# Optimization experiments

Hardware: AMD Instinct MI355X
Metric: run time of the kernel (lower is better)

The kernel has to match this reference:

```python
import jax, jax.numpy as jnp
import numpy as np

INPUT_SIZE = 64
HIDDEN = 1024
SEQ_LEN = 256
BATCH = 128
TARGET_LEN = 96


def lstm_cell(x, h, c, Wih, Whh, bih, bhh):
    # x: [B, in], h/c: [B, H]; torch gate order: i, f, g, o
    z = x @ Wih.T + h @ Whh.T + bih + bhh  # [B, 4H]
    i, f, g, o = jnp.split(z, 4, axis=-1)
    c_new = jax.nn.sigmoid(f) * c + jax.nn.sigmoid(i) * jnp.tanh(g)
    h_new = jax.nn.sigmoid(o) * jnp.tanh(c_new)
    return h_new, c_new


def setup_inputs() -> dict:
    key = jax.random.key(0)
    ks = jax.random.split(key, 12)
    s_in = 1.0 / np.sqrt(HIDDEN)  # torch LSTM init scale ~ U(-1/sqrt(H), 1/sqrt(H))
    def u(k, shape):
        return jax.random.uniform(k, shape, jnp.float32, -s_in, s_in)
    return {
        "input_batch": jax.random.normal(ks[0], (SEQ_LEN, BATCH, INPUT_SIZE), jnp.float32),
        "target_batch": jax.random.normal(ks[1], (TARGET_LEN, BATCH, INPUT_SIZE), jnp.float32),
        "enc_Wih": u(ks[2], (4 * HIDDEN, INPUT_SIZE)),
        "enc_Whh": u(ks[3], (4 * HIDDEN, HIDDEN)),
        "enc_bih": u(ks[4], (4 * HIDDEN,)),
        "enc_bhh": u(ks[5], (4 * HIDDEN,)),
        "dec_Wih": u(ks[6], (4 * HIDDEN, INPUT_SIZE)),
        "dec_Whh": u(ks[7], (4 * HIDDEN, HIDDEN)),
        "dec_bih": u(ks[8], (4 * HIDDEN,)),
        "dec_bhh": u(ks[9], (4 * HIDDEN,)),
        "lin_W": u(ks[10], (INPUT_SIZE, HIDDEN)),
        "lin_b": u(ks[11], (INPUT_SIZE,)),
    }


def reference(input_batch, target_batch, enc_Wih, enc_Whh, enc_bih, enc_bhh,
              dec_Wih, dec_Whh, dec_bih, dec_bhh, lin_W, lin_b):
    B = input_batch.shape[1]
    h0 = jnp.zeros((B, HIDDEN), input_batch.dtype)
    c0 = jnp.zeros((B, HIDDEN), input_batch.dtype)

    # ---- encoder: LSTM over seq_len ----
    def enc_step(carry, x_t):
        h, c = carry
        h, c = lstm_cell(x_t, h, c, enc_Wih, enc_Whh, enc_bih, enc_bhh)
        return (h, c), None
    (h_enc, c_enc), _ = jax.lax.scan(enc_step, (h0, c0), input_batch)

    # ---- decoder: recursive (no teacher forcing), target_len steps ----
    def dec_step(carry, _):
        x, h, c = carry
        h, c = lstm_cell(x, h, c, dec_Wih, dec_Whh, dec_bih, dec_bhh)
        y = h @ lin_W.T + lin_b  # [B, input_size]
        return (y, h, c), y
    x0 = input_batch[-1]  # [B, input_size]
    _, outputs = jax.lax.scan(dec_step, (x0, h_enc, c_enc), None, length=TARGET_LEN)
    return outputs  # [target_len, B, input_size]
```

## Files before the change

### kernel.cpp

```cpp
#include <hip/hip_runtime.h>
#include <stdint.h>

#define IN    64
#define H     1024
#define G4    4096
#define BATCH 128
#define SEQ   256
#define TLEN  96
#define KCAT  1088
#define NSTEP (SEQ + TLEN)
#define NBLK  256
#define HPAD  1032
#define ZPAD  132

typedef __attribute__((ext_vector_type(8))) short bf16x8;
typedef __attribute__((ext_vector_type(4))) float f32x4;

__device__ __forceinline__ unsigned short f2bf(float f) {
  union { float f; uint32_t u; } v; v.f = f;
  uint32_t u = v.u;
  return (unsigned short)((u + 0x7fffu + ((u >> 16) & 1u)) >> 16);
}

__device__ __forceinline__ void gload_lds16_sc0(const unsigned short* g, unsigned short* l) {
  __builtin_amdgcn_global_load_lds((const __attribute__((address_space(1))) unsigned int*)g,
                                   (__attribute__((address_space(3))) unsigned int*)l, 16, 0, 1);
}

__global__ void k_convert(const float* __restrict__ src, unsigned short* __restrict__ dst, int n) {
  int i = blockIdx.x * blockDim.x + threadIdx.x;
  int stride = gridDim.x * blockDim.x;
  for (; i < n; i += stride) dst[i] = f2bf(src[i]);
}

__global__ void k_pack(const float* __restrict__ Wih, const float* __restrict__ Whh,
                       const float* __restrict__ bih, const float* __restrict__ bhh,
                       unsigned short* __restrict__ Wcat, float* __restrict__ bcat) {
  int p = blockIdx.x;
  int j = p >> 2, g = p & 3;
  int r = g * H + j;
  for (int c = threadIdx.x; c < KCAT; c += blockDim.x) {
    float v = (c < IN) ? Wih[r * IN + c] : Whh[r * H + (c - IN)];
    Wcat[(size_t)p * KCAT + c] = f2bf(v);
  }
  if (threadIdx.x == 0) bcat[p] = bih[r] + bhh[r];
}

__global__ void k_deceff(const float* __restrict__ Wih, const float* __restrict__ Whh,
                         const float* __restrict__ bih, const float* __restrict__ bhh,
                         const float* __restrict__ lin, const float* __restrict__ linb,
                         unsigned short* __restrict__ Weff, float* __restrict__ beff) {
  int p = blockIdx.x;
  int j = p >> 2, g = p & 3;
  int r = g * H + j;
  __shared__ float wr[IN];
  if (threadIdx.x < IN) wr[threadIdx.x] = Wih[r * IN + threadIdx.x];
  __syncthreads();
  for (int k = threadIdx.x; k < H; k += blockDim.x) {
    float acc = Whh[(size_t)r * H + k];
    #pragma unroll 8
    for (int i = 0; i < IN; ++i) acc += wr[i] * lin[(size_t)i * H + k];
    Weff[(size_t)p * H + k] = f2bf(acc);
  }
  if (threadIdx.x == 0) {
    float s = bih[r] + bhh[r];
    for (int i = 0; i < IN; ++i) s += wr[i] * linb[i];
    beff[p] = s;
  }
}

__global__ __launch_bounds__(512, 2) void k_lstm(
    const unsigned short* __restrict__ xin,
    const unsigned short* __restrict__ Wenc,  const float* __restrict__ benc,
    const unsigned short* __restrict__ Wdec0, const float* __restrict__ bdec0,
    const unsigned short* __restrict__ Wdeff, const float* __restrict__ bdeff,
    unsigned short* __restrict__ hbuf, unsigned short* __restrict__ hhist,
    unsigned int* __restrict__ flags, unsigned int* __restrict__ tickets)
{
  extern __shared__ char smem[];
  unsigned short* hs = (unsigned short*)smem;
  float*          zs = (float*)(smem + 16 * HPAD * 2);
  __shared__ int s_xcd, s_slot;
  const int tid  = threadIdx.x;
  const int lane = tid & 63;
  const int wave = tid >> 6;
  if (tid == 0) {
    unsigned x;
    asm volatile("s_getreg_b32 %0, hwreg(HW_REG_XCC_ID)" : "=s"(x));
    x &= 7;
    unsigned tk = __hip_atomic_fetch_add(&tickets[x], 1u, __ATOMIC_RELAXED, __HIP_MEMORY_SCOPE_AGENT);
    s_xcd = (int)x; s_slot = (int)(tk & 31);
  }
  __syncthreads();
  const int grp  = s_xcd;
  const int slot = s_slot;
  const int m0   = grp * 16;
  const int n0   = slot * 128;
  const int gw   = n0 + wave * 16;
  const int fm   = lane & 15;
  const int fk   = (lane >> 4) * 8;
  const int crow = tid >> 5;
  const int ul   = tid & 31;
  const unsigned int* myflags = flags + (size_t)grp * 32;

  bf16x8 B[34];
  float cst = 0.f;
  int p = 0;
  for (int t = 0; t < NSTEP; ++t) {
    const bool is_enc = (t < SEQ);
    if (t == 0 || t == SEQ) {
      const unsigned short* W = (t == 0) ? Wenc : Wdec0;
      const unsigned short* wr = W + (size_t)(gw + fm) * KCAT + fk;
      #pragma unroll
      for (int kt = 0; kt < 32; ++kt) B[kt] = *(const bf16x8*)(wr + IN + kt * 32);
      B[32] = *(const bf16x8*)(wr);
      B[33] = *(const bf16x8*)(wr + 32);
    } else if (t == SEQ + 1) {
      const unsigned short* wr = Wdeff + (size_t)(gw + fm) * H + fk;
      #pragma unroll
      for (int kt = 0; kt < 32; ++kt) B[kt] = *(const bf16x8*)(wr + kt * 32);
    }
    const float* bias = is_enc ? benc : (t == SEQ ? bdec0 : bdeff);
    const unsigned short* xsrc =
        is_enc ? xin + (size_t)t * BATCH * IN
               : (t == SEQ ? xin + (size_t)(SEQ - 1) * BATCH * IN : nullptr);
    if (t > 0) {
      const unsigned short* hb = hbuf + (size_t)p * BATCH * H + (size_t)m0 * H;
      #pragma unroll
      for (int j = 0; j < 4; ++j) {
        int row  = wave * 2 + (j >> 1);
        int half = (j & 1) * 512;
        gload_lds16_sc0(hb + (size_t)row * H + half + lane * 8, &hs[row * HPAD + half]);
      }
    }
    __syncthreads();
    f32x4 acc = {0.f, 0.f, 0.f, 0.f};
    if (t > 0) {
      const unsigned short* as = &hs[fm * HPAD + fk];
      #pragma unroll
      for (int kt = 0; kt < 32; ++kt)
        acc = __builtin_amdgcn_mfma_f32_16x16x32_bf16(*(const bf16x8*)(as + kt * 32), B[kt], acc, 0, 0, 0);
    }
    if (xsrc) {
      const unsigned short* xa = xsrc + (size_t)(m0 + fm) * IN + fk;
      acc = __builtin_amdgcn_mfma_f32_16x16x32_bf16(*(const bf16x8*)(xa),      B[32], acc, 0, 0, 0);
      acc = __builtin_amdgcn_mfma_f32_16x16x32_bf16(*(const bf16x8*)(xa + 32), B[33], acc, 0, 0, 0);
    }
    {
      int colz = wave * 16 + fm;
      int rb   = (lane >> 4) * 4;
      #pragma unroll
      for (int j = 0; j < 4; ++j) zs[(rb + j) * ZPAD + colz] = acc[j];
    }
    __syncthreads();
    {
      const float4 z4 = *(const float4*)&zs[crow * ZPAD + 4 * ul];
      const float4 b4 = *(const float4*)&bias[n0 + 4 * ul];
      float zi = z4.x + b4.x, zf = z4.y + b4.y, zg = z4.z + b4.z, zo = z4.w + b4.w;
      float gi = 1.f / (1.f + __expf(-zi));
      float gf = 1.f / (1.f + __expf(-zf));
      float gg = tanhf(zg);
      float go = 1.f / (1.f + __expf(-zo));
      float c  = gf * cst + gi * gg;
      cst = c;
      float h = go * tanhf(c);
      unsigned short hb16 = f2bf(h);
      size_t idx = (size_t)(m0 + crow) * H + (n0 >> 2) + ul;
      hbuf[(size_t)(1 - p) * BATCH * H + idx] = hb16;
      if (!is_enc) hhist[(size_t)(t - SEQ) * BATCH * H + idx] = hb16;
    }
    p ^= 1;
    if (t + 1 < NSTEP) {
      __syncthreads();
      if (tid == 0)
        __hip_atomic_store(&flags[grp * 32 + slot], (unsigned)(t + 1),
                           __ATOMIC_RELAXED, __HIP_MEMORY_SCOPE_AGENT);
      if (tid < 32) {
        while (__hip_atomic_load(&myflags[tid], __ATOMIC_RELAXED, __HIP_MEMORY_SCOPE_AGENT) < (unsigned)(t + 1))
          __builtin_amdgcn_s_sleep(1);
      }
      __syncthreads();
    }
  }
}

__global__ __launch_bounds__(256) void k_out(
    const unsigned short* __restrict__ hhist, const unsigned short* __restrict__ linb16,
    const float* __restrict__ linb, float* __restrict__ out)
{
  const int tid  = threadIdx.x;
  const int lane = tid & 63;
  const int wave = tid >> 6;
  const int fm   = lane & 15;
  const int fk   = (lane >> 4) * 8;
  const int R0   = blockIdx.x * 64 + wave * 16;
  f32x4 acc[4] = {{0.f,0.f,0.f,0.f},{0.f,0.f,0.f,0.f},{0.f,0.f,0.f,0.f},{0.f,0.f,0.f,0.f}};
  const unsigned short* ha = hhist + (size_t)(R0 + fm) * H + fk;
  #pragma unroll 2
  for (int kc = 0; kc < H; kc += 32) {
    bf16x8 a = *(const bf16x8*)(ha + kc);
    #pragma unroll
    for (int nq = 0; nq < 4; ++nq) {
      bf16x8 b = *(const bf16x8*)(linb16 + (size_t)(nq * 16 + fm) * H + fk + kc);
      acc[nq] = __builtin_amdgcn_mfma_f32_16x16x32_bf16(a, b, acc[nq], 0, 0, 0);
    }
  }
  #pragma unroll
  for (int nq = 0; nq < 4; ++nq) {
    int col = nq * 16 + fm;
    float bb = linb[col];
    #pragma unroll
    for (int j = 0; j < 4; ++j) {
      int R = R0 + (lane >> 4) * 4 + j;
      out[(size_t)R * IN + col] = acc[nq][j] + bb;
    }
  }
}

extern "C" void kernel_launch(void* const* d_in, const int* in_sizes, int n_in,
                              void* d_out, int out_size, void* d_ws, size_t ws_size,
                              hipStream_t stream) {
  const float* input_batch = (const float*)d_in[0];
  const float* eWih = (const float*)d_in[2];
  const float* eWhh = (const float*)d_in[3];
  const float* ebih = (const float*)d_in[4];
  const float* ebhh = (const float*)d_in[5];
  const float* dWih = (const float*)d_in[6];
  const float* dWhh = (const float*)d_in[7];
  const float* dbih = (const float*)d_in[8];
  const float* dbhh = (const float*)d_in[9];
  const float* linW = (const float*)d_in[10];
  const float* linb = (const float*)d_in[11];
  float* out = (float*)d_out;

  char* ws = (char*)d_ws;
  size_t off = 0;
  auto alloc = [&](size_t bytes) -> void* {
    void* pp = ws + off;
    off = (off + bytes + 255) & ~(size_t)255;
    return pp;
  };
  unsigned short* xin   = (unsigned short*)alloc((size_t)SEQ * BATCH * IN * 2);
  unsigned short* Wenc  = (unsigned short*)alloc((size_t)G4 * KCAT * 2);
  float*          benc  = (float*)         alloc((size_t)G4 * 4);
  unsigned short* Wdec0 = (unsigned short*)alloc((size_t)G4 * KCAT * 2);
  float*          bdec0 = (float*)         alloc((size_t)G4 * 4);
  unsigned short* Wdeff = (unsigned short*)alloc((size_t)G4 * H * 2);
  float*          bdeff = (float*)         alloc((size_t)G4 * 4);
  unsigned short* linbf = (unsigned short*)alloc((size_t)IN * H * 2);
  unsigned short* hbuf  = (unsigned short*)alloc((size_t)2 * BATCH * H * 2);
  unsigned short* hhist = (unsigned short*)alloc((size_t)TLEN * BATCH * H * 2);
  unsigned int*   flags = (unsigned int*)  alloc((size_t)8 * 32 * sizeof(unsigned));
  unsigned int*   tickets = (unsigned int*)alloc((size_t)8 * sizeof(unsigned));
  (void)ws_size; (void)in_sizes; (void)n_in; (void)out_size;

  hipMemsetAsync(flags, 0, (size_t)8 * 32 * sizeof(unsigned), stream);
  hipMemsetAsync(tickets, 0, (size_t)8 * sizeof(unsigned), stream);
  hipLaunchKernelGGL(k_convert, dim3(512), dim3(256), 0, stream, input_batch, xin, SEQ * BATCH * IN);
  hipLaunchKernelGGL(k_convert, dim3(64),  dim3(256), 0, stream, linW, linbf, IN * H);
  hipLaunchKernelGGL(k_pack,   dim3(G4), dim3(256), 0, stream, eWih, eWhh, ebih, ebhh, Wenc, benc);
  hipLaunchKernelGGL(k_pack,   dim3(G4), dim3(256), 0, stream, dWih, dWhh, dbih, dbhh, Wdec0, bdec0);
  hipLaunchKernelGGL(k_deceff, dim3(G4), dim3(256), 0, stream, dWih, dWhh, dbih, dbhh, linW, linb, Wdeff, bdeff);

  void* args[] = { &xin, &Wenc, &benc, &Wdec0, &bdec0, &Wdeff, &bdeff, &hbuf, &hhist, &flags, &tickets };
  hipLaunchCooperativeKernel((void*)k_lstm, dim3(NBLK), dim3(512), args, 86016, stream);

  hipLaunchKernelGGL(k_out, dim3((TLEN * BATCH) / 64), dim3(256), 0, stream, hhist, linbf, linb, out);
}
```

Measured before the change: 4.322 ms.

## Swap MFMA operands so each lane holds all four gates, drop z LDS staging

```diff
diff --git a/kernel.cpp b/kernel.cpp
--- a/kernel.cpp
+++ b/kernel.cpp
@@ -11,7 +11,6 @@
 #define NSTEP (SEQ + TLEN)
 #define NBLK  256
 #define HPAD  1032
-#define ZPAD  132
 
 typedef __attribute__((ext_vector_type(8))) short bf16x8;
 typedef __attribute__((ext_vector_type(4))) float f32x4;
@@ -79,7 +78,7 @@
 {
   extern __shared__ char smem[];
   unsigned short* hs = (unsigned short*)smem;
-  float*          zs = (float*)(smem + 16 * HPAD * 2);
+  __shared__ unsigned short ht[16][40];
   __shared__ int s_xcd, s_slot;
   const int tid  = threadIdx.x;
   const int lane = tid & 63;
@@ -98,12 +97,15 @@
   const int n0   = slot * 128;
   const int gw   = n0 + wave * 16;
   const int fm   = lane & 15;
-  const int fk   = (lane >> 4) * 8;
-  const int crow = tid >> 5;
-  const int ul   = tid & 31;
+  const int fku  = lane >> 4;
+  const int fk   = fku * 8;
+  const int unit = slot * 32 + wave * 4 + fku;
+  const int hrow = tid >> 5;
+  const int hcol = tid & 31;
   const unsigned int* myflags = flags + (size_t)grp * 32;
 
   bf16x8 B[34];
+  float4 bias4;
   float cst = 0.f;
   int p = 0;
   for (int t = 0; t < NSTEP; ++t) {
@@ -120,7 +122,10 @@
       #pragma unroll
       for (int kt = 0; kt < 32; ++kt) B[kt] = *(const bf16x8*)(wr + kt * 32);
     }
-    const float* bias = is_enc ? benc : (t == SEQ ? bdec0 : bdeff);
+    if (t == 0 || t == SEQ || t == SEQ + 1) {
+      const float* bptr = (t == 0) ? benc : (t == SEQ ? bdec0 : bdeff);
+      bias4 = *(const float4*)&bptr[4 * unit];
+    }
     const unsigned short* xsrc =
         is_enc ? xin + (size_t)t * BATCH * IN
                : (t == SEQ ? xin + (size_t)(SEQ - 1) * BATCH * IN : nullptr);
@@ -134,29 +139,26 @@
       }
     }
     __syncthreads();
-    f32x4 acc = {0.f, 0.f, 0.f, 0.f};
+    f32x4 acc0 = {0.f, 0.f, 0.f, 0.f};
+    f32x4 acc1 = {0.f, 0.f, 0.f, 0.f};
     if (t > 0) {
       const unsigned short* as = &hs[fm * HPAD + fk];
       #pragma unroll
-      for (int kt = 0; kt < 32; ++kt)
-        acc = __builtin_amdgcn_mfma_f32_16x16x32_bf16(*(const bf16x8*)(as + kt * 32), B[kt], acc, 0, 0, 0);
+      for (int kt = 0; kt < 32; kt += 2) {
+        acc0 = __builtin_amdgcn_mfma_f32_16x16x32_bf16(B[kt],     *(const bf16x8*)(as + kt * 32),      acc0, 0, 0, 0);
+        acc1 = __builtin_amdgcn_mfma_f32_16x16x32_bf16(B[kt + 1], *(const bf16x8*)(as + kt * 32 + 32), acc1, 0, 0, 0);
+      }
     }
     if (xsrc) {
       const unsigned short* xa = xsrc + (size_t)(m0 + fm) * IN + fk;
-      acc = __builtin_amdgcn_mfma_f32_16x16x32_bf16(*(const bf16x8*)(xa),      B[32], acc, 0, 0, 0);
-      acc = __builtin_amdgcn_mfma_f32_16x16x32_bf16(*(const bf16x8*)(xa + 32), B[33], acc, 0, 0, 0);
+      acc0 = __builtin_amdgcn_mfma_f32_16x16x32_bf16(B[32], *(const bf16x8*)(xa),      acc0, 0, 0, 0);
+      acc1 = __builtin_amdgcn_mfma_f32_16x16x32_bf16(B[33], *(const bf16x8*)(xa + 32), acc1, 0, 0, 0);
     }
     {
-      int colz = wave * 16 + fm;
-      int rb   = (lane >> 4) * 4;
-      #pragma unroll
-      for (int j = 0; j < 4; ++j) zs[(rb + j) * ZPAD + colz] = acc[j];
-    }
-    __syncthreads();
-    {
-      const float4 z4 = *(const float4*)&zs[crow * ZPAD + 4 * ul];
-      const float4 b4 = *(const float4*)&bias[n0 + 4 * ul];
-      float zi = z4.x + b4.x, zf = z4.y + b4.y, zg = z4.z + b4.z, zo = z4.w + b4.w;
+      float zi = acc0[0] + acc1[0] + bias4.x;
+      float zf = acc0[1] + acc1[1] + bias4.y;
+      float zg = acc0[2] + acc1[2] + bias4.z;
+      float zo = acc0[3] + acc1[3] + bias4.w;
       float gi = 1.f / (1.f + __expf(-zi));
       float gf = 1.f / (1.f + __expf(-zf));
       float gg = tanhf(zg);
@@ -164,10 +166,14 @@
       float c  = gf * cst + gi * gg;
       cst = c;
       float h = go * tanhf(c);
-      unsigned short hb16 = f2bf(h);
-      size_t idx = (size_t)(m0 + crow) * H + (n0 >> 2) + ul;
-      hbuf[(size_t)(1 - p) * BATCH * H + idx] = hb16;
-      if (!is_enc) hhist[(size_t)(t - SEQ) * BATCH * H + idx] = hb16;
+      ht[fm][(wave << 2) + fku] = f2bf(h);
+    }
+    __syncthreads();
+    {
+      unsigned short hv = ht[hrow][hcol];
+      size_t idx = (size_t)(m0 + hrow) * H + (size_t)slot * 32 + hcol;
+      hbuf[(size_t)(1 - p) * BATCH * H + idx] = hv;
+      if (!is_enc) hhist[(size_t)(t - SEQ) * BATCH * H + idx] = hv;
     }
     p ^= 1;
     if (t + 1 < NSTEP) {
```

Result: faster. 3.984 ms (-7.8%).
